# Kernel optimization log

Measured on AMD Instinct MI355X. Metric: run time of the kernel, lower is better.

The kernel has to match this reference:

```python
import jax, jax.numpy as jnp
import numpy as np

NEG_SLOPE = 0.2  # PyG GATConv default LeakyReLU slope


def gat_layer(x, src, dst, W, a_src, a_dst, bias, heads, out_dim, concat, n_nodes):
    # x: [N, F_in]; W: [F_in, heads*out_dim]
    h = (x @ W).reshape(n_nodes, heads, out_dim)          # [N, H, C]
    alpha_src = jnp.sum(h * a_src, axis=-1)               # [N, H]
    alpha_dst = jnp.sum(h * a_dst, axis=-1)               # [N, H]
    e = jax.nn.leaky_relu(alpha_src[src] + alpha_dst[dst], NEG_SLOPE)  # [E, H]
    # softmax over edges grouped by destination node (self-loops guarantee nonempty segments)
    m = jax.ops.segment_max(e, dst, num_segments=n_nodes)  # [N, H]
    w = jnp.exp(e - m[dst])
    s = jax.ops.segment_sum(w, dst, num_segments=n_nodes)  # [N, H]
    alpha = w / s[dst]                                     # [E, H]
    msg = h[src] * alpha[:, :, None]                       # [E, H, C]
    out = jax.ops.segment_sum(msg, dst, num_segments=n_nodes)  # [N, H, C]
    if concat:
        out = out.reshape(n_nodes, heads * out_dim)
    else:
        out = out.mean(axis=1)
    return out + bias


def setup_inputs() -> dict:
    key = jax.random.key(0)
    ks = jax.random.split(key, 12)
    N, E = 50000, 600000
    F_IN, OUT = 256, 64
    H1, C1 = 2, 2 * OUT          # conv1: heads=2, per-head dim 128
    F2 = H1 * C1                 # 256
    x = jax.random.normal(ks[0], (N, F_IN), dtype=jnp.float32)
    edge_index = jax.random.randint(ks[1], (2, E), 0, N, dtype=jnp.int64)
    g1 = 1.0 / np.sqrt(F_IN)
    g2 = 1.0 / np.sqrt(F2)
    return {
        "x": x,
        "edge_index": edge_index,
        "W1": jax.random.normal(ks[2], (F_IN, H1 * C1), dtype=jnp.float32) * g1,
        "a1_src": jax.random.normal(ks[3], (H1, C1), dtype=jnp.float32) * g2,
        "a1_dst": jax.random.normal(ks[4], (H1, C1), dtype=jnp.float32) * g2,
        "b1": jnp.zeros((H1 * C1,), dtype=jnp.float32),
        "W2": jax.random.normal(ks[5], (F2, OUT), dtype=jnp.float32) * g2,
        "a2_src": jax.random.normal(ks[6], (1, OUT), dtype=jnp.float32) * 0.1,
        "a2_dst": jax.random.normal(ks[7], (1, OUT), dtype=jnp.float32) * 0.1,
        "b2": jnp.zeros((OUT,), dtype=jnp.float32),
    }


def reference(x, edge_index, W1, a1_src, a1_dst, b1, W2, a2_src, a2_dst, b2):
    N = x.shape[0]
    # add self-loops (PyG GATConv default)
    loops = jnp.arange(N, dtype=edge_index.dtype)
    src = jnp.concatenate([edge_index[0], loops])
    dst = jnp.concatenate([edge_index[1], loops])
    OUT = W2.shape[1]
    h = gat_layer(x, src, dst, W1, a1_src, a1_dst, b1,
                  heads=2, out_dim=2 * OUT, concat=True, n_nodes=N)
    h = jax.nn.elu(h)
    out = gat_layer(h, src, dst, W2, a2_src, a2_dst, b2,
                    heads=1, out_dim=OUT, concat=False, n_nodes=N)
    return out
```

## Files before the change

kernel.cpp:

```cpp
#include <hip/hip_runtime.h>
#include <hip/hip_bf16.h>
#include <math.h>


#define NSLOPE 0.2f

using bf16x8 = __attribute__((ext_vector_type(8))) short;
using f32x4  = __attribute__((ext_vector_type(4))) float;
using u16x8  = __attribute__((ext_vector_type(8))) unsigned short;
using u16x4  = __attribute__((ext_vector_type(4))) unsigned short;

__device__ __forceinline__ unsigned short bf16_rne(float f) {
    unsigned u = __float_as_uint(f);
    return (unsigned short)((u + 0x7FFFu + ((u >> 16) & 1u)) >> 16);
}
__device__ __forceinline__ float bf16_to_f(unsigned short h) {
    return __uint_as_float(((unsigned)h) << 16);
}

__global__ __launch_bounds__(256) void k_prep_all(const float* __restrict__ x,
                                                  const float* __restrict__ W1,
                                                  const float* __restrict__ W2,
                                                  const int* __restrict__ edst,
                                                  unsigned short* __restrict__ Xhi,
                                                  unsigned short* __restrict__ W1hi,
                                                  unsigned short* __restrict__ W2hi,
                                                  int* __restrict__ deg,
                                                  int BX, int total4, int E) {
    int b = blockIdx.x, t = threadIdx.x;
    if (b < BX) {
        int id = b * 256 + t;
        if (id >= total4) return;
        float4 v = *(const float4*)&x[(size_t)id * 4];
        unsigned short hi[4];
        hi[0] = bf16_rne(v.x); hi[1] = bf16_rne(v.y);
        hi[2] = bf16_rne(v.z); hi[3] = bf16_rne(v.w);
        *(u16x4*)&Xhi[(size_t)id * 4] = *(u16x4*)hi;
    } else if (b < BX + 64) {
        int id = (b - BX) * 256 + t;
        int n = id >> 6, kg = id & 63;
        unsigned short hi[4];
#pragma unroll
        for (int c = 0; c < 4; ++c) {
            float w = W1[(kg * 4 + c) * 256 + n];
            hi[c] = bf16_rne(w);
        }
        *(u16x4*)&W1hi[n * 256 + kg * 4] = *(u16x4*)hi;
    } else if (b < BX + 128) {
        int id = (b - BX - 64) * 256 + t;
        int n = id >> 8, k = id & 255;
        W2hi[n * 256 + k] = bf16_rne(W2[k * 64 + n]);
    } else {
        int i = (b - BX - 128) * 256 + t;
        if (i < E) atomicAdd(&deg[edst[i]], 1);
    }
}

__global__ __launch_bounds__(256) void k_scan_ab(const int* __restrict__ deg,
                                                 int* __restrict__ part,
                                                 int* __restrict__ ticket,
                                                 int* __restrict__ off_n,
                                                 int n, int CH) {
    __shared__ int sd[256];
    __shared__ int lastflag;
    int b = blockIdx.x, t = threadIdx.x;
    int s = b * CH, e = min(n, s + CH);
    int loc = 0;
    for (int i = s + t; i < e; i += 256) loc += deg[i] + 1;
    sd[t] = loc;
    __syncthreads();
    for (int o = 128; o > 0; o >>= 1) {
        if (t < o) sd[t] += sd[t + o];
        __syncthreads();
    }
    if (t == 0) {
        part[b] = sd[0];
        __threadfence();
        int old = atomicAdd(ticket, 1);
        lastflag = (old == (int)gridDim.x - 1);
    }
    __syncthreads();
    if (lastflag) {
        __threadfence();
        int v = ((volatile int*)part)[t];
        sd[t] = v;
        __syncthreads();
        for (int o = 1; o < 256; o <<= 1) {
            int u = (t >= o) ? sd[t - o] : 0;
            __syncthreads();
            sd[t] += u;
            __syncthreads();
        }
        part[t] = sd[t] - v;
        if (t == 255) *off_n = sd[255];
    }
}

__global__ __launch_bounds__(256) void k_scan_c(const int* __restrict__ deg,
                                                const int* __restrict__ part,
                                                int* __restrict__ off,
                                                int* __restrict__ cur,
                                                int* __restrict__ srcl, int n, int CH) {
    __shared__ int sd[256];
    int b = blockIdx.x, t = threadIdx.x;
    int s = b * CH, e = min(n, s + CH);
    int base = part[b];
    for (int c = s; c < e; c += 256) {
        int i = c + t;
        int v = (i < e) ? (deg[i] + 1) : 0;
        sd[t] = v;
        __syncthreads();
        for (int o = 1; o < 256; o <<= 1) {
            int u = (t >= o) ? sd[t - o] : 0;
            __syncthreads();
            sd[t] += u;
            __syncthreads();
        }
        if (i < e) {
            int ex = base + sd[t] - v;
            off[i] = ex;
            cur[i] = ex + 1;
            srcl[ex] = i;
        }
        base += sd[255];
        __syncthreads();
    }
}

__global__ void k_fill(const int* __restrict__ src, const int* __restrict__ dst,
                       int* cur, int* __restrict__ srcl, int E) {
    int i = blockIdx.x * blockDim.x + threadIdx.x;
    if (i >= E) return;
    int s = src[i], d = dst[i];
    int p = atomicAdd(&cur[d], 1);
    srcl[p] = s;
}

#define G1S 40
__global__ __launch_bounds__(256) void k_gemm1(const unsigned short* __restrict__ Xhi,
                                               const unsigned short* __restrict__ Whi,
                                               const float* __restrict__ a1s,
                                               const float* __restrict__ a1d,
                                               unsigned short* __restrict__ h1b,
                                               float* __restrict__ as_,
                                               float* __restrict__ ad_, int M) {
    __shared__ unsigned short sAh[128 * G1S];
    __shared__ unsigned short sBh[128 * G1S];
    __shared__ float salS[128][2], salD[128][2];
    int t = threadIdx.x;
    int lane = t & 63, wave = t >> 6;
    int q = lane >> 4, m = lane & 15;
    int row0 = blockIdx.x * 128;
    int head = blockIdx.y;
    int col0 = head * 128;
    int rbase = (wave & 1) * 64, cbase = (wave >> 1) * 64;
    f32x4 acc[4][4];
#pragma unroll
    for (int i = 0; i < 4; ++i)
#pragma unroll
        for (int j = 0; j < 4; ++j) acc[i][j] = (f32x4){0.f, 0.f, 0.f, 0.f};

    for (int kc = 0; kc < 256; kc += 32) {
#pragma unroll
        for (int i2 = 0; i2 < 2; ++i2) {
            int slot = t + i2 * 256;
            int r = slot >> 2, kg = slot & 3;
            int row = row0 + r;
            u16x8 vh = {0, 0, 0, 0, 0, 0, 0, 0};
            if (row < M) vh = *(const u16x8*)&Xhi[(size_t)row * 256 + kc + kg * 8];
            *(u16x8*)&sAh[r * G1S + kg * 8] = vh;
        }
#pragma unroll
        for (int i2 = 0; i2 < 2; ++i2) {
            int slot = t + i2 * 256;
            int n = slot >> 2, kg = slot & 3;
            *(u16x8*)&sBh[n * G1S + kg * 8] =
                *(const u16x8*)&Whi[(size_t)(col0 + n) * 256 + kc + kg * 8];
        }
        __syncthreads();
        bf16x8 ah[4], bh[4];
#pragma unroll
        for (int i = 0; i < 4; ++i)
            ah[i] = *(bf16x8*)&sAh[(rbase + i * 16 + m) * G1S + q * 8];
#pragma unroll
        for (int j = 0; j < 4; ++j)
            bh[j] = *(bf16x8*)&sBh[(cbase + j * 16 + m) * G1S + q * 8];
#pragma unroll
        for (int i = 0; i < 4; ++i)
#pragma unroll
            for (int j = 0; j < 4; ++j)
                acc[i][j] = __builtin_amdgcn_mfma_f32_16x16x32_bf16(ah[i], bh[j], acc[i][j], 0, 0, 0);
        __syncthreads();
    }
    float sv[4], dv[4];
#pragma unroll
    for (int j = 0; j < 4; ++j) {
        sv[j] = a1s[head * 128 + cbase + j * 16 + m];
        dv[j] = a1d[head * 128 + cbase + j * 16 + m];
    }
#pragma unroll
    for (int i = 0; i < 4; ++i) {
#pragma unroll
        for (int r = 0; r < 4; ++r) {
            int rl = rbase + i * 16 + q * 4 + r;
            int row = row0 + rl;
            float ps = acc[i][0][r] * sv[0] + acc[i][1][r] * sv[1]
                     + acc[i][2][r] * sv[2] + acc[i][3][r] * sv[3];
            float pd = acc[i][0][r] * dv[0] + acc[i][1][r] * dv[1]
                     + acc[i][2][r] * dv[2] + acc[i][3][r] * dv[3];
#pragma unroll
            for (int mask = 1; mask < 16; mask <<= 1) {
                ps += __shfl_xor(ps, mask, 64);
                pd += __shfl_xor(pd, mask, 64);
            }
            if (m == 0) {
                salS[rl][cbase >> 6] = ps;
                salD[rl][cbase >> 6] = pd;
            }
            if (row < M) {
#pragma unroll
                for (int j = 0; j < 4; ++j)
                    h1b[(size_t)row * 256 + col0 + cbase + j * 16 + m] = bf16_rne(acc[i][j][r]);
            }
        }
    }
    __syncthreads();
    if (t < 128) {
        int row = row0 + t;
        if (row < M) {
            as_[row * 2 + head] = salS[t][0] + salS[t][1];
            ad_[row * 2 + head] = salD[t][0] + salD[t][1];
        }
    }
}

__global__ __launch_bounds__(256) void k_agg1(const unsigned short* __restrict__ h1b,
                                              const float* __restrict__ as,
                                              const float* __restrict__ ad,
                                              const int* __restrict__ off,
                                              const int* __restrict__ srcl,
                                              const float* __restrict__ b1,
                                              unsigned short* __restrict__ helu_b, int N) {
    int wid = (blockIdx.x * blockDim.x + threadIdx.x) >> 6;
    int lane = threadIdx.x & 63;
    if (wid >= N) return;
    int p0 = off[wid], p1 = off[wid + 1];
    float ad0 = ad[wid * 2], ad1 = ad[wid * 2 + 1];
    int half = lane >> 5, hl = lane & 31;
    int headL = hl >> 4;
    float acc[8];
#pragma unroll
    for (int c = 0; c < 8; ++c) acc[c] = 0.f;
    float sumw = 0.f;
    for (int base = p0; base < p1; base += 64) {
        int p = base + lane;
        int cnt = min(64, p1 - base);
        int s = 0; float w0 = 0.f, w1 = 0.f;
        if (p < p1) {
            s = srcl[p];
            float2 av = *(const float2*)&as[s * 2];
            float l0 = av.x + ad0; l0 = l0 >= 0.f ? l0 : NSLOPE * l0;
            float l1 = av.y + ad1; l1 = l1 >= 0.f ? l1 : NSLOPE * l1;
            w0 = __expf(l0); w1 = __expf(l1);
        }
        int pairs = (cnt + 1) >> 1;
        int jj = 0;
        for (; jj + 2 <= pairs; jj += 2) {
            int e0 = 2 * jj + half, e1 = e0 + 2;
            int sa = __shfl(s, e0, 64), sb = __shfl(s, e1, 64);
            float wa0 = __shfl(w0, e0, 64), wa1 = __shfl(w1, e0, 64);
            float wb0 = __shfl(w0, e1, 64), wb1 = __shfl(w1, e1, 64);
            u16x8 hva = *(const u16x8*)&h1b[(size_t)sa * 256 + hl * 8];
            u16x8 hvb = *(const u16x8*)&h1b[(size_t)sb * 256 + hl * 8];
            float wa = headL ? wa1 : wa0;
            float wb = headL ? wb1 : wb0;
            sumw += wa + wb;
#pragma unroll
            for (int c = 0; c < 8; ++c)
                acc[c] += wa * bf16_to_f(hva[c]) + wb * bf16_to_f(hvb[c]);
        }
        for (; jj < pairs; ++jj) {
            int e0 = 2 * jj + half;
            int sa = __shfl(s, e0, 64);
            float wa0 = __shfl(w0, e0, 64), wa1 = __shfl(w1, e0, 64);
            u16x8 hva = *(const u16x8*)&h1b[(size_t)sa * 256 + hl * 8];
            float wa = headL ? wa1 : wa0;
            sumw += wa;
#pragma unroll
            for (int c = 0; c < 8; ++c) acc[c] += wa * bf16_to_f(hva[c]);
        }
    }
#pragma unroll
    for (int c = 0; c < 8; ++c) acc[c] += __shfl_xor(acc[c], 32, 64);
    sumw += __shfl_xor(sumw, 32, 64);
    float inv = 1.0f / sumw;
    int ch = hl * 8 + half * 4;
    float4 bv = *(const float4*)&b1[ch];
    float bb[4] = {bv.x, bv.y, bv.z, bv.w};
    unsigned short o[4];
#pragma unroll
    for (int c = 0; c < 4; ++c) {
        float v = acc[half * 4 + c] * inv + bb[c];
        v = v > 0.f ? v : expm1f(v);
        o[c] = bf16_rne(v);
    }
    *(u16x4*)&helu_b[(size_t)wid * 256 + ch] = *(u16x4*)o;
}

__global__ __launch_bounds__(256) void k_gemm2(const unsigned short* __restrict__ hb,
                                               const unsigned short* __restrict__ Whi,
                                               const float* __restrict__ a2s,
                                               const float* __restrict__ a2d,
                                               unsigned short* __restrict__ h2b,
                                               float* __restrict__ as_,
                                               float* __restrict__ ad_, int M) {
    __shared__ unsigned short sA[128 * G1S];
    __shared__ unsigned short sBh[64 * G1S];
    int t = threadIdx.x;
    int lane = t & 63, wave = t >> 6;
    int q = lane >> 4, m = lane & 15;
    int row0 = blockIdx.x * 128;
    int rbase = wave * 32;
    f32x4 acc[2][4];
#pragma unroll
    for (int i = 0; i < 2; ++i)
#pragma unroll
        for (int j = 0; j < 4; ++j) acc[i][j] = (f32x4){0.f, 0.f, 0.f, 0.f};

    for (int kc = 0; kc < 256; kc += 32) {
#pragma unroll
        for (int i = 0; i < 2; ++i) {
            int slot = t + i * 256;
            int r = slot >> 2, kg = slot & 3;
            int row = row0 + r;
            u16x8 v = {0, 0, 0, 0, 0, 0, 0, 0};
            if (row < M) v = *(const u16x8*)&hb[(size_t)row * 256 + kc + kg * 8];
            *(u16x8*)&sA[r * G1S + kg * 8] = v;
        }
        {
            int n = t >> 2, kg = t & 3;
            *(u16x8*)&sBh[n * G1S + kg * 8] =
                *(const u16x8*)&Whi[(size_t)n * 256 + kc + kg * 8];
        }
        __syncthreads();
        bf16x8 a[2], bh[4];
#pragma unroll
        for (int i = 0; i < 2; ++i)
            a[i] = *(bf16x8*)&sA[(rbase + i * 16 + m) * G1S + q * 8];
#pragma unroll
        for (int j = 0; j < 4; ++j)
            bh[j] = *(bf16x8*)&sBh[(j * 16 + m) * G1S + q * 8];
#pragma unroll
        for (int i = 0; i < 2; ++i)
#pragma unroll
            for (int j = 0; j < 4; ++j)
                acc[i][j] = __builtin_amdgcn_mfma_f32_16x16x32_bf16(a[i], bh[j], acc[i][j], 0, 0, 0);
        __syncthreads();
    }
    float sv[4], dv[4];
#pragma unroll
    for (int j = 0; j < 4; ++j) {
        sv[j] = a2s[j * 16 + m];
        dv[j] = a2d[j * 16 + m];
    }
#pragma unroll
    for (int i = 0; i < 2; ++i) {
#pragma unroll
        for (int r = 0; r < 4; ++r) {
            int row = row0 + rbase + i * 16 + q * 4 + r;
            float ps = acc[i][0][r] * sv[0] + acc[i][1][r] * sv[1]
                     + acc[i][2][r] * sv[2] + acc[i][3][r] * sv[3];
            float pd = acc[i][0][r] * dv[0] + acc[i][1][r] * dv[1]
                     + acc[i][2][r] * dv[2] + acc[i][3][r] * dv[3];
#pragma unroll
            for (int mask = 1; mask < 16; mask <<= 1) {
                ps += __shfl_xor(ps, mask, 64);
                pd += __shfl_xor(pd, mask, 64);
            }
            if (row < M) {
#pragma unroll
                for (int j = 0; j < 4; ++j)
                    h2b[(size_t)row * 64 + j * 16 + m] = bf16_rne(acc[i][j][r]);
                if (m == 0) { as_[row] = ps; ad_[row] = pd; }
            }
        }
    }
}

__global__ __launch_bounds__(256) void k_agg2(const unsigned short* __restrict__ h2b,
                                              const float* __restrict__ as,
                                              const float* __restrict__ ad,
                                              const int* __restrict__ off,
                                              const int* __restrict__ srcl,
                                              const float* __restrict__ b2,
                                              float* __restrict__ out, int N) {
    int wid = (blockIdx.x * blockDim.x + threadIdx.x) >> 6;
    int lane = threadIdx.x & 63;
    if (wid >= N) return;
    int p0 = off[wid], p1 = off[wid + 1];
    float adw = ad[wid];
    int g = lane >> 4, gl = lane & 15;
    float acc[4];
#pragma unroll
    for (int c = 0; c < 4; ++c) acc[c] = 0.f;
    float sumw = 0.f;
    for (int base = p0; base < p1; base += 64) {
        int p = base + lane;
        int cnt = min(64, p1 - base);
        int s = 0; float w = 0.f;
        if (p < p1) {
            s = srcl[p];
            float l = as[s] + adw;
            l = l >= 0.f ? l : NSLOPE * l;
            w = __expf(l);
        }
        int quads = (cnt + 3) >> 2;
        int jj = 0;
        for (; jj + 2 <= quads; jj += 2) {
            int e0 = 4 * jj + g, e1 = e0 + 4;
            int sa = __shfl(s, e0, 64), sb = __shfl(s, e1, 64);
            float wa = __shfl(w, e0, 64), wb = __shfl(w, e1, 64);
            u16x4 hva = *(const u16x4*)&h2b[(size_t)sa * 64 + gl * 4];
            u16x4 hvb = *(const u16x4*)&h2b[(size_t)sb * 64 + gl * 4];
            sumw += wa + wb;
            acc[0] += wa * bf16_to_f(hva.x) + wb * bf16_to_f(hvb.x);
            acc[1] += wa * bf16_to_f(hva.y) + wb * bf16_to_f(hvb.y);
            acc[2] += wa * bf16_to_f(hva.z) + wb * bf16_to_f(hvb.z);
            acc[3] += wa * bf16_to_f(hva.w) + wb * bf16_to_f(hvb.w);
        }
        for (; jj < quads; ++jj) {
            int e0 = 4 * jj + g;
            int sa = __shfl(s, e0, 64);
            float wa = __shfl(w, e0, 64);
            u16x4 hva = *(const u16x4*)&h2b[(size_t)sa * 64 + gl * 4];
            sumw += wa;
            acc[0] += wa * bf16_to_f(hva.x);
            acc[1] += wa * bf16_to_f(hva.y);
            acc[2] += wa * bf16_to_f(hva.z);
            acc[3] += wa * bf16_to_f(hva.w);
        }
    }
#pragma unroll
    for (int c = 0; c < 4; ++c) {
        acc[c] += __shfl_xor(acc[c], 16, 64);
        acc[c] += __shfl_xor(acc[c], 32, 64);
    }
    sumw += __shfl_xor(sumw, 16, 64);
    sumw += __shfl_xor(sumw, 32, 64);
    if (g == 0) {
        float inv = 1.0f / sumw;
        float4 bv = *(const float4*)&b2[gl * 4];
        float4 o;
        o.x = acc[0] * inv + bv.x;
        o.y = acc[1] * inv + bv.y;
        o.z = acc[2] * inv + bv.z;
        o.w = acc[3] * inv + bv.w;
        *(float4*)&out[(size_t)wid * 64 + gl * 4] = o;
    }
}

extern "C" void kernel_launch(void* const* d_in, const int* in_sizes, int n_in,
                              void* d_out, int out_size, void* d_ws, size_t ws_size,
                              hipStream_t stream) {
    if (n_in < 10) return;
    const float* x   = (const float*)d_in[0];
    const int*   ei  = (const int*)d_in[1];
    const float* W1  = (const float*)d_in[2];
    const float* a1s = (const float*)d_in[3];
    const float* a1d = (const float*)d_in[4];
    const float* b1  = (const float*)d_in[5];
    const float* W2  = (const float*)d_in[6];
    const float* a2s = (const float*)d_in[7];
    const float* a2d = (const float*)d_in[8];
    const float* b2  = (const float*)d_in[9];
    float* out = (float*)d_out;

    const int N = in_sizes[0] / 256;
    const int E = in_sizes[1] / 2;
    const int T = E + N;
    const int* esrc = ei;
    const int* edst = ei + E;

    char* ws = (char*)d_ws;
    size_t o = 0;
    auto alloc = [&](size_t bytes) -> void* {
        void* p = ws + o;
        o = (o + bytes + 255) & ~(size_t)255;
        return p;
    };
    size_t szX = (size_t)N * 256 * 2;
    char* regionA = (char*)alloc(szX);
    unsigned short* Xhi    = (unsigned short*)regionA;
    unsigned short* helu_b = (unsigned short*)regionA;

    unsigned short* h1b  = (unsigned short*)alloc((size_t)N * 256 * 2);
    unsigned short* W1hi = (unsigned short*)alloc(256 * 256 * 2);
    unsigned short* W2hi = (unsigned short*)alloc(64 * 256 * 2);
    unsigned short* h2b  = (unsigned short*)alloc((size_t)N * 64 * 2);
    float* al1s = (float*)alloc((size_t)N * 2 * 4);
    float* al1d = (float*)alloc((size_t)N * 2 * 4);
    float* al2s = (float*)alloc((size_t)N * 4);
    float* al2d = (float*)alloc((size_t)N * 4);
    int* deg  = (int*)alloc((size_t)(N + 64) * 4);
    int* ticket = deg + N;
    int* off  = (int*)alloc((size_t)(N + 1) * 4);
    int* cur  = (int*)alloc((size_t)N * 4);
    int* part = (int*)alloc(256 * 4);
    int* srcl = (int*)alloc((size_t)T * 4);
    if (o > ws_size) return;

    const int CH = (N + 255) / 256;
    const int total4 = N * 64;
    const int BX = (total4 + 255) / 256;
    const int BH = (E + 255) / 256;

    hipMemsetAsync(deg, 0, (size_t)(N + 64) * 4, stream);
    k_prep_all<<<BX + 128 + BH, 256, 0, stream>>>(x, W1, W2, edst, Xhi,
                                                  W1hi, W2hi, deg,
                                                  BX, total4, E);
    k_scan_ab<<<256, 256, 0, stream>>>(deg, part, ticket, &off[N], N, CH);
    k_scan_c<<<256, 256, 0, stream>>>(deg, part, off, cur, srcl, N, CH);
    k_fill<<<(E + 255) / 256, 256, 0, stream>>>(esrc, edst, cur, srcl, E);

    dim3 g1((N + 127) / 128, 2);
    k_gemm1<<<g1, 256, 0, stream>>>(Xhi, W1hi, a1s, a1d, h1b, al1s, al1d, N);
    k_agg1<<<(N + 3) / 4, 256, 0, stream>>>(h1b, al1s, al1d, off, srcl, b1, helu_b, N);

    k_gemm2<<<(N + 127) / 128, 256, 0, stream>>>(helu_b, W2hi, a2s, a2d,
                                                 h2b, al2s, al2d, N);
    k_agg2<<<(N + 3) / 4, 256, 0, stream>>>(h2b, al2s, al2d, off, srcl, b2, out, N);
}
```

Baseline: 287.7 us.

## Fuse graph preprocessing stages into one cooperative kernel with grid syncs

Replaces the memset, prep, two-phase scan and fill kernels with a single cooperative kernel of 1024 blocks that uses grid-wide barriers between stages. The goal is to cut launch overhead and inter-kernel gaps in the CSR build. In exchange, each stage runs grid-stride loops on a fixed grid and pays for grid syncs, and the block-level scan phases use only 256 of the 1024 blocks.

```diff
diff --git a/kernel.cpp b/kernel.cpp
--- a/kernel.cpp
+++ b/kernel.cpp
@@ -1,6 +1,9 @@
 #include <hip/hip_runtime.h>
 #include <hip/hip_bf16.h>
+#include <hip/hip_cooperative_groups.h>
 #include <math.h>
+
+namespace cg = cooperative_groups;
 
 
 #define NSLOPE 0.2f
@@ -18,72 +21,67 @@
     return __uint_as_float(((unsigned)h) << 16);
 }
 
-__global__ __launch_bounds__(256) void k_prep_all(const float* __restrict__ x,
-                                                  const float* __restrict__ W1,
-                                                  const float* __restrict__ W2,
-                                                  const int* __restrict__ edst,
-                                                  unsigned short* __restrict__ Xhi,
-                                                  unsigned short* __restrict__ W1hi,
-                                                  unsigned short* __restrict__ W2hi,
-                                                  int* __restrict__ deg,
-                                                  int BX, int total4, int E) {
+__global__ __launch_bounds__(256) void k_graph(const float* __restrict__ x,
+                                               const float* __restrict__ W1,
+                                               const float* __restrict__ W2,
+                                               const int* __restrict__ esrc,
+                                               const int* __restrict__ edst,
+                                               unsigned short* __restrict__ Xhi,
+                                               unsigned short* __restrict__ W1hi,
+                                               unsigned short* __restrict__ W2hi,
+                                               int* __restrict__ deg,
+                                               int* __restrict__ part,
+                                               int* __restrict__ off,
+                                               int* __restrict__ cur,
+                                               int* __restrict__ srcl,
+                                               int N, int E, int total4, int CH) {
+    cg::grid_group gg = cg::this_grid();
+    __shared__ int sd[256];
     int b = blockIdx.x, t = threadIdx.x;
-    if (b < BX) {
-        int id = b * 256 + t;
-        if (id >= total4) return;
+    int tid = b * 256 + t;
+    int nthr = gridDim.x * 256;
+
+    for (int i = tid; i < N; i += nthr) deg[i] = 0;
+    for (int id = tid; id < total4; id += nthr) {
         float4 v = *(const float4*)&x[(size_t)id * 4];
         unsigned short hi[4];
         hi[0] = bf16_rne(v.x); hi[1] = bf16_rne(v.y);
         hi[2] = bf16_rne(v.z); hi[3] = bf16_rne(v.w);
         *(u16x4*)&Xhi[(size_t)id * 4] = *(u16x4*)hi;
-    } else if (b < BX + 64) {
-        int id = (b - BX) * 256 + t;
+    }
+    for (int id = tid; id < 16384; id += nthr) {
         int n = id >> 6, kg = id & 63;
         unsigned short hi[4];
 #pragma unroll
-        for (int c = 0; c < 4; ++c) {
-            float w = W1[(kg * 4 + c) * 256 + n];
-            hi[c] = bf16_rne(w);
-        }
+        for (int c = 0; c < 4; ++c) hi[c] = bf16_rne(W1[(kg * 4 + c) * 256 + n]);
         *(u16x4*)&W1hi[n * 256 + kg * 4] = *(u16x4*)hi;
-    } else if (b < BX + 128) {
-        int id = (b - BX - 64) * 256 + t;
+    }
+    for (int id = tid; id < 16384; id += nthr) {
         int n = id >> 8, k = id & 255;
         W2hi[n * 256 + k] = bf16_rne(W2[k * 64 + n]);
-    } else {
-        int i = (b - BX - 128) * 256 + t;
-        if (i < E) atomicAdd(&deg[edst[i]], 1);
-    }
-}
-
-__global__ __launch_bounds__(256) void k_scan_ab(const int* __restrict__ deg,
-                                                 int* __restrict__ part,
-                                                 int* __restrict__ ticket,
-                                                 int* __restrict__ off_n,
-                                                 int n, int CH) {
-    __shared__ int sd[256];
-    __shared__ int lastflag;
-    int b = blockIdx.x, t = threadIdx.x;
-    int s = b * CH, e = min(n, s + CH);
-    int loc = 0;
-    for (int i = s + t; i < e; i += 256) loc += deg[i] + 1;
-    sd[t] = loc;
-    __syncthreads();
-    for (int o = 128; o > 0; o >>= 1) {
-        if (t < o) sd[t] += sd[t + o];
-        __syncthreads();
-    }
-    if (t == 0) {
-        part[b] = sd[0];
-        __threadfence();
-        int old = atomicAdd(ticket, 1);
-        lastflag = (old == (int)gridDim.x - 1);
-    }
-    __syncthreads();
-    if (lastflag) {
-        __threadfence();
-        int v = ((volatile int*)part)[t];
-        sd[t] = v;
+    }
+    gg.sync();
+
+    for (int i = tid; i < E; i += nthr) atomicAdd(&deg[edst[i]], 1);
+    gg.sync();
+
+    if (b < 256) {
+        int s = b * CH, e = min(N, s + CH);
+        int loc = 0;
+        for (int i = s + t; i < e; i += 256) loc += deg[i] + 1;
+        sd[t] = loc;
+        __syncthreads();
+        for (int o = 128; o > 0; o >>= 1) {
+            if (t < o) sd[t] += sd[t + o];
+            __syncthreads();
+        }
+        if (t == 0) part[b] = sd[0];
+    }
+    gg.sync();
+
+    if (b < 256) {
+        int pb = part[b];
+        sd[t] = part[t];
         __syncthreads();
         for (int o = 1; o < 256; o <<= 1) {
             int u = (t >= o) ? sd[t - o] : 0;
@@ -91,49 +89,38 @@
             sd[t] += u;
             __syncthreads();
         }
-        part[t] = sd[t] - v;
-        if (t == 255) *off_n = sd[255];
-    }
-}
-
-__global__ __launch_bounds__(256) void k_scan_c(const int* __restrict__ deg,
-                                                const int* __restrict__ part,
-                                                int* __restrict__ off,
-                                                int* __restrict__ cur,
-                                                int* __restrict__ srcl, int n, int CH) {
-    __shared__ int sd[256];
-    int b = blockIdx.x, t = threadIdx.x;
-    int s = b * CH, e = min(n, s + CH);
-    int base = part[b];
-    for (int c = s; c < e; c += 256) {
-        int i = c + t;
-        int v = (i < e) ? (deg[i] + 1) : 0;
-        sd[t] = v;
-        __syncthreads();
-        for (int o = 1; o < 256; o <<= 1) {
-            int u = (t >= o) ? sd[t - o] : 0;
+        int base = sd[b] - pb;
+        if (b == 0 && t == 0) off[N] = sd[255];
+        __syncthreads();
+        int s = b * CH, e = min(N, s + CH);
+        for (int c = s; c < e; c += 256) {
+            int i = c + t;
+            int vv = (i < e) ? (deg[i] + 1) : 0;
+            sd[t] = vv;
             __syncthreads();
-            sd[t] += u;
+            for (int o = 1; o < 256; o <<= 1) {
+                int u = (t >= o) ? sd[t - o] : 0;
+                __syncthreads();
+                sd[t] += u;
+                __syncthreads();
+            }
+            if (i < e) {
+                int ex = base + sd[t] - vv;
+                off[i] = ex;
+                cur[i] = ex + 1;
+                srcl[ex] = i;
+            }
+            base += sd[255];
             __syncthreads();
         }
-        if (i < e) {
-            int ex = base + sd[t] - v;
-            off[i] = ex;
-            cur[i] = ex + 1;
-            srcl[ex] = i;
-        }
-        base += sd[255];
-        __syncthreads();
-    }
-}
-
-__global__ void k_fill(const int* __restrict__ src, const int* __restrict__ dst,
-                       int* cur, int* __restrict__ srcl, int E) {
-    int i = blockIdx.x * blockDim.x + threadIdx.x;
-    if (i >= E) return;
-    int s = src[i], d = dst[i];
-    int p = atomicAdd(&cur[d], 1);
-    srcl[p] = s;
+    }
+    gg.sync();
+
+    for (int i = tid; i < E; i += nthr) {
+        int s = esrc[i], d = edst[i];
+        int p = atomicAdd(&cur[d], 1);
+        srcl[p] = s;
+    }
 }
 
 #define G1S 40
@@ -502,7 +489,6 @@
     float* al2s = (float*)alloc((size_t)N * 4);
     float* al2d = (float*)alloc((size_t)N * 4);
     int* deg  = (int*)alloc((size_t)(N + 64) * 4);
-    int* ticket = deg + N;
     int* off  = (int*)alloc((size_t)(N + 1) * 4);
     int* cur  = (int*)alloc((size_t)N * 4);
     int* part = (int*)alloc(256 * 4);
@@ -511,16 +497,16 @@
 
     const int CH = (N + 255) / 256;
     const int total4 = N * 64;
-    const int BX = (total4 + 255) / 256;
-    const int BH = (E + 255) / 256;
-
-    hipMemsetAsync(deg, 0, (size_t)(N + 64) * 4, stream);
-    k_prep_all<<<BX + 128 + BH, 256, 0, stream>>>(x, W1, W2, edst, Xhi,
-                                                  W1hi, W2hi, deg,
-                                                  BX, total4, E);
-    k_scan_ab<<<256, 256, 0, stream>>>(deg, part, ticket, &off[N], N, CH);
-    k_scan_c<<<256, 256, 0, stream>>>(deg, part, off, cur, srcl, N, CH);
-    k_fill<<<(E + 255) / 256, 256, 0, stream>>>(esrc, edst, cur, srcl, E);
+
+    {
+        int N_ = N, E_ = E, total4_ = total4, CH_ = CH;
+        void* args[] = {(void*)&x, (void*)&W1, (void*)&W2, (void*)&esrc, (void*)&edst,
+                        (void*)&Xhi, (void*)&W1hi, (void*)&W2hi,
+                        (void*)&deg, (void*)&part, (void*)&off, (void*)&cur, (void*)&srcl,
+                        (void*)&N_, (void*)&E_, (void*)&total4_, (void*)&CH_};
+        hipLaunchCooperativeKernel((const void*)k_graph, dim3(1024), dim3(256),
+                                   args, 0, stream);
+    }
 
     dim3 g1((N + 127) / 128, 2);
     k_gemm1<<<g1, 256, 0, stream>>>(Xhi, W1hi, a1s, a1d, h1b, al1s, al1d, N);
```

After: 717.2 us. 149% more time.

## Fuse CSR scan and edge fill into one kernel with grid barriers

Applied to the files above, without the earlier changes.

Merges the three CSR-building kernels (block partial sums, offset scan, edge fill) into a single persistent 256-block kernel that uses a software grid barrier built on an atomic counter between phases. Each block redoes the small 256-entry prefix scan itself instead of relying on a last-block ticket. The goal is to cut two kernel launches and their inter-kernel gaps. In exchange, correctness depends on all 256 blocks being co-resident, and the fill phase now runs a grid-stride loop over edges with only 65536 threads.

```diff
diff --git a/kernel.cpp b/kernel.cpp
--- a/kernel.cpp
+++ b/kernel.cpp
@@ -56,15 +56,31 @@
     }
 }
 
-__global__ __launch_bounds__(256) void k_scan_ab(const int* __restrict__ deg,
-                                                 int* __restrict__ part,
-                                                 int* __restrict__ ticket,
-                                                 int* __restrict__ off_n,
-                                                 int n, int CH) {
+__device__ __forceinline__ void gbar256(int* bar, int phase) {
+    __syncthreads();
+    if (threadIdx.x == 0) {
+        __hip_atomic_fetch_add(bar, 1, __ATOMIC_ACQ_REL, __HIP_MEMORY_SCOPE_AGENT);
+        while (__hip_atomic_load(bar, __ATOMIC_ACQUIRE, __HIP_MEMORY_SCOPE_AGENT)
+               < 256 * phase) {
+            __builtin_amdgcn_s_sleep(8);
+        }
+    }
+    __syncthreads();
+}
+
+__global__ __launch_bounds__(256) void k_scanfill(const int* __restrict__ deg,
+                                                  const int* __restrict__ esrc,
+                                                  const int* __restrict__ edst,
+                                                  int* __restrict__ part,
+                                                  int* __restrict__ bar,
+                                                  int* __restrict__ off,
+                                                  int* __restrict__ cur,
+                                                  int* __restrict__ srcl,
+                                                  int N, int E, int CH) {
     __shared__ int sd[256];
-    __shared__ int lastflag;
     int b = blockIdx.x, t = threadIdx.x;
-    int s = b * CH, e = min(n, s + CH);
+    int s = b * CH, e = min(N, s + CH);
+
     int loc = 0;
     for (int i = s + t; i < e; i += 256) loc += deg[i] + 1;
     sd[t] = loc;
@@ -73,17 +89,35 @@
         if (t < o) sd[t] += sd[t + o];
         __syncthreads();
     }
-    if (t == 0) {
-        part[b] = sd[0];
-        __threadfence();
-        int old = atomicAdd(ticket, 1);
-        lastflag = (old == (int)gridDim.x - 1);
-    }
-    __syncthreads();
-    if (lastflag) {
-        __threadfence();
-        int v = ((volatile int*)part)[t];
-        sd[t] = v;
+    if (t == 0)
+        __hip_atomic_store(&part[b], sd[0], __ATOMIC_RELEASE, __HIP_MEMORY_SCOPE_AGENT);
+    gbar256(bar, 1);
+
+    int pb = __hip_atomic_load(&part[t], __ATOMIC_ACQUIRE, __HIP_MEMORY_SCOPE_AGENT);
+    sd[t] = pb;
+    __syncthreads();
+    for (int o = 1; o < 256; o <<= 1) {
+        int u = (t >= o) ? sd[t - o] : 0;
+        __syncthreads();
+        sd[t] += u;
+        __syncthreads();
+    }
+    int base = sd[b];
+    int total = sd[255];
+    __syncthreads();
+    if (t == 0) sd[0] = base;
+    __syncthreads();
+    int own;
+    {
+        own = __hip_atomic_load(&part[b], __ATOMIC_ACQUIRE, __HIP_MEMORY_SCOPE_AGENT);
+    }
+    base = sd[0] - own;
+    if (b == 0 && t == 0) off[N] = total;
+    __syncthreads();
+    for (int c = s; c < e; c += 256) {
+        int i = c + t;
+        int vv = (i < e) ? (deg[i] + 1) : 0;
+        sd[t] = vv;
         __syncthreads();
         for (int o = 1; o < 256; o <<= 1) {
             int u = (t >= o) ? sd[t - o] : 0;
@@ -91,33 +125,8 @@
             sd[t] += u;
             __syncthreads();
         }
-        part[t] = sd[t] - v;
-        if (t == 255) *off_n = sd[255];
-    }
-}
-
-__global__ __launch_bounds__(256) void k_scan_c(const int* __restrict__ deg,
-                                                const int* __restrict__ part,
-                                                int* __restrict__ off,
-                                                int* __restrict__ cur,
-                                                int* __restrict__ srcl, int n, int CH) {
-    __shared__ int sd[256];
-    int b = blockIdx.x, t = threadIdx.x;
-    int s = b * CH, e = min(n, s + CH);
-    int base = part[b];
-    for (int c = s; c < e; c += 256) {
-        int i = c + t;
-        int v = (i < e) ? (deg[i] + 1) : 0;
-        sd[t] = v;
-        __syncthreads();
-        for (int o = 1; o < 256; o <<= 1) {
-            int u = (t >= o) ? sd[t - o] : 0;
-            __syncthreads();
-            sd[t] += u;
-            __syncthreads();
-        }
         if (i < e) {
-            int ex = base + sd[t] - v;
+            int ex = base + sd[t] - vv;
             off[i] = ex;
             cur[i] = ex + 1;
             srcl[ex] = i;
@@ -125,15 +134,14 @@
         base += sd[255];
         __syncthreads();
     }
-}
-
-__global__ void k_fill(const int* __restrict__ src, const int* __restrict__ dst,
-                       int* cur, int* __restrict__ srcl, int E) {
-    int i = blockIdx.x * blockDim.x + threadIdx.x;
-    if (i >= E) return;
-    int s = src[i], d = dst[i];
-    int p = atomicAdd(&cur[d], 1);
-    srcl[p] = s;
+    gbar256(bar, 2);
+
+    int tid = b * 256 + t, nthr = 256 * 256;
+    for (int i = tid; i < E; i += nthr) {
+        int ss = esrc[i], d = edst[i];
+        int p = atomicAdd(&cur[d], 1);
+        srcl[p] = ss;
+    }
 }
 
 #define G1S 40
@@ -502,7 +510,7 @@
     float* al2s = (float*)alloc((size_t)N * 4);
     float* al2d = (float*)alloc((size_t)N * 4);
     int* deg  = (int*)alloc((size_t)(N + 64) * 4);
-    int* ticket = deg + N;
+    int* bar  = deg + N;
     int* off  = (int*)alloc((size_t)(N + 1) * 4);
     int* cur  = (int*)alloc((size_t)N * 4);
     int* part = (int*)alloc(256 * 4);
@@ -518,9 +526,8 @@
     k_prep_all<<<BX + 128 + BH, 256, 0, stream>>>(x, W1, W2, edst, Xhi,
                                                   W1hi, W2hi, deg,
                                                   BX, total4, E);
-    k_scan_ab<<<256, 256, 0, stream>>>(deg, part, ticket, &off[N], N, CH);
-    k_scan_c<<<256, 256, 0, stream>>>(deg, part, off, cur, srcl, N, CH);
-    k_fill<<<(E + 255) / 256, 256, 0, stream>>>(esrc, edst, cur, srcl, E);
+    k_scanfill<<<256, 256, 0, stream>>>(deg, esrc, edst, part, bar,
+                                        off, cur, srcl, N, E, CH);
 
     dim3 g1((N + 127) / 128, 2);
     k_gemm1<<<g1, 256, 0, stream>>>(Xhi, W1hi, a1s, a1d, h1b, al1s, al1d, N);
```

Result: slower. 328.5 us (+14.2%).

## Compute both heads per GEMM1 block and unroll aggregation loops by four

Applied to the files above, without the earlier changes.

GEMM1 now computes all 256 output columns (both heads) in one block, with each wave covering 64 rows by 128 columns of one head. This halves the grid, avoids reading the X tile twice, and drops the cross-wave sum of attention logits. The cost is a doubled accumulator array (128 floats per lane) and larger B staging in LDS, which raises register pressure and may lower occupancy. Both aggregation kernels also gain a 4-edge unrolled gather loop so more independent row loads are in flight.

```diff
diff --git a/kernel.cpp b/kernel.cpp
--- a/kernel.cpp
+++ b/kernel.cpp
@@ -145,20 +145,20 @@
                                                float* __restrict__ as_,
                                                float* __restrict__ ad_, int M) {
     __shared__ unsigned short sAh[128 * G1S];
-    __shared__ unsigned short sBh[128 * G1S];
+    __shared__ unsigned short sBh[256 * G1S];
     __shared__ float salS[128][2], salD[128][2];
     int t = threadIdx.x;
     int lane = t & 63, wave = t >> 6;
     int q = lane >> 4, m = lane & 15;
     int row0 = blockIdx.x * 128;
-    int head = blockIdx.y;
-    int col0 = head * 128;
-    int rbase = (wave & 1) * 64, cbase = (wave >> 1) * 64;
-    f32x4 acc[4][4];
+    int rbase = (wave & 1) * 64;
+    int head = wave >> 1;
+    int cbase = head * 128;
+    f32x4 acc[4][8];
 #pragma unroll
     for (int i = 0; i < 4; ++i)
 #pragma unroll
-        for (int j = 0; j < 4; ++j) acc[i][j] = (f32x4){0.f, 0.f, 0.f, 0.f};
+        for (int j = 0; j < 8; ++j) acc[i][j] = (f32x4){0.f, 0.f, 0.f, 0.f};
 
     for (int kc = 0; kc < 256; kc += 32) {
 #pragma unroll
@@ -171,32 +171,32 @@
             *(u16x8*)&sAh[r * G1S + kg * 8] = vh;
         }
 #pragma unroll
-        for (int i2 = 0; i2 < 2; ++i2) {
+        for (int i2 = 0; i2 < 4; ++i2) {
             int slot = t + i2 * 256;
             int n = slot >> 2, kg = slot & 3;
             *(u16x8*)&sBh[n * G1S + kg * 8] =
-                *(const u16x8*)&Whi[(size_t)(col0 + n) * 256 + kc + kg * 8];
-        }
-        __syncthreads();
-        bf16x8 ah[4], bh[4];
+                *(const u16x8*)&Whi[(size_t)n * 256 + kc + kg * 8];
+        }
+        __syncthreads();
+        bf16x8 ah[4], bh[8];
 #pragma unroll
         for (int i = 0; i < 4; ++i)
             ah[i] = *(bf16x8*)&sAh[(rbase + i * 16 + m) * G1S + q * 8];
 #pragma unroll
-        for (int j = 0; j < 4; ++j)
+        for (int j = 0; j < 8; ++j)
             bh[j] = *(bf16x8*)&sBh[(cbase + j * 16 + m) * G1S + q * 8];
 #pragma unroll
         for (int i = 0; i < 4; ++i)
 #pragma unroll
-            for (int j = 0; j < 4; ++j)
+            for (int j = 0; j < 8; ++j)
                 acc[i][j] = __builtin_amdgcn_mfma_f32_16x16x32_bf16(ah[i], bh[j], acc[i][j], 0, 0, 0);
         __syncthreads();
     }
-    float sv[4], dv[4];
-#pragma unroll
-    for (int j = 0; j < 4; ++j) {
-        sv[j] = a1s[head * 128 + cbase + j * 16 + m];
-        dv[j] = a1d[head * 128 + cbase + j * 16 + m];
+    float sv[8], dv[8];
+#pragma unroll
+    for (int j = 0; j < 8; ++j) {
+        sv[j] = a1s[cbase + j * 16 + m];
+        dv[j] = a1d[cbase + j * 16 + m];
     }
 #pragma unroll
     for (int i = 0; i < 4; ++i) {
@@ -204,23 +204,25 @@
         for (int r = 0; r < 4; ++r) {
             int rl = rbase + i * 16 + q * 4 + r;
             int row = row0 + rl;
-            float ps = acc[i][0][r] * sv[0] + acc[i][1][r] * sv[1]
-                     + acc[i][2][r] * sv[2] + acc[i][3][r] * sv[3];
-            float pd = acc[i][0][r] * dv[0] + acc[i][1][r] * dv[1]
-                     + acc[i][2][r] * dv[2] + acc[i][3][r] * dv[3];
+            float ps = 0.f, pd = 0.f;
+#pragma unroll
+            for (int j = 0; j < 8; ++j) {
+                ps += acc[i][j][r] * sv[j];
+                pd += acc[i][j][r] * dv[j];
+            }
 #pragma unroll
             for (int mask = 1; mask < 16; mask <<= 1) {
                 ps += __shfl_xor(ps, mask, 64);
                 pd += __shfl_xor(pd, mask, 64);
             }
             if (m == 0) {
-                salS[rl][cbase >> 6] = ps;
-                salD[rl][cbase >> 6] = pd;
+                salS[rl][head] = ps;
+                salD[rl][head] = pd;
             }
             if (row < M) {
 #pragma unroll
-                for (int j = 0; j < 4; ++j)
-                    h1b[(size_t)row * 256 + col0 + cbase + j * 16 + m] = bf16_rne(acc[i][j][r]);
+                for (int j = 0; j < 8; ++j)
+                    h1b[(size_t)row * 256 + cbase + j * 16 + m] = bf16_rne(acc[i][j][r]);
             }
         }
     }
@@ -228,8 +230,10 @@
     if (t < 128) {
         int row = row0 + t;
         if (row < M) {
-            as_[row * 2 + head] = salS[t][0] + salS[t][1];
-            ad_[row * 2 + head] = salD[t][0] + salD[t][1];
+            as_[row * 2 + 0] = salS[t][0];
+            as_[row * 2 + 1] = salS[t][1];
+            ad_[row * 2 + 0] = salD[t][0];
+            ad_[row * 2 + 1] = salD[t][1];
         }
     }
 }
@@ -265,6 +269,28 @@
         }
         int pairs = (cnt + 1) >> 1;
         int jj = 0;
+        for (; jj + 4 <= pairs; jj += 4) {
+            int e0 = 2 * jj + half, e1 = e0 + 2, e2 = e0 + 4, e3 = e0 + 6;
+            int sa = __shfl(s, e0, 64), sb = __shfl(s, e1, 64);
+            int sc = __shfl(s, e2, 64), se = __shfl(s, e3, 64);
+            float wa0 = __shfl(w0, e0, 64), wa1 = __shfl(w1, e0, 64);
+            float wb0 = __shfl(w0, e1, 64), wb1 = __shfl(w1, e1, 64);
+            float wc0 = __shfl(w0, e2, 64), wc1 = __shfl(w1, e2, 64);
+            float wd0 = __shfl(w0, e3, 64), wd1 = __shfl(w1, e3, 64);
+            u16x8 hva = *(const u16x8*)&h1b[(size_t)sa * 256 + hl * 8];
+            u16x8 hvb = *(const u16x8*)&h1b[(size_t)sb * 256 + hl * 8];
+            u16x8 hvc = *(const u16x8*)&h1b[(size_t)sc * 256 + hl * 8];
+            u16x8 hvd = *(const u16x8*)&h1b[(size_t)se * 256 + hl * 8];
+            float wa = headL ? wa1 : wa0;
+            float wb = headL ? wb1 : wb0;
+            float wc = headL ? wc1 : wc0;
+            float wd = headL ? wd1 : wd0;
+            sumw += (wa + wb) + (wc + wd);
+#pragma unroll
+            for (int c = 0; c < 8; ++c)
+                acc[c] += (wa * bf16_to_f(hva[c]) + wb * bf16_to_f(hvb[c]))
+                        + (wc * bf16_to_f(hvc[c]) + wd * bf16_to_f(hvd[c]));
+        }
         for (; jj + 2 <= pairs; jj += 2) {
             int e0 = 2 * jj + half, e1 = e0 + 2;
             int sa = __shfl(s, e0, 64), sb = __shfl(s, e1, 64);
@@ -416,6 +442,26 @@
         }
         int quads = (cnt + 3) >> 2;
         int jj = 0;
+        for (; jj + 4 <= quads; jj += 4) {
+            int e0 = 4 * jj + g, e1 = e0 + 4, e2 = e0 + 8, e3 = e0 + 12;
+            int sa = __shfl(s, e0, 64), sb = __shfl(s, e1, 64);
+            int sc = __shfl(s, e2, 64), se = __shfl(s, e3, 64);
+            float wa = __shfl(w, e0, 64), wb = __shfl(w, e1, 64);
+            float wc = __shfl(w, e2, 64), wd = __shfl(w, e3, 64);
+            u16x4 hva = *(const u16x4*)&h2b[(size_t)sa * 64 + gl * 4];
+            u16x4 hvb = *(const u16x4*)&h2b[(size_t)sb * 64 + gl * 4];
+            u16x4 hvc = *(const u16x4*)&h2b[(size_t)sc * 64 + gl * 4];
+            u16x4 hvd = *(const u16x4*)&h2b[(size_t)se * 64 + gl * 4];
+            sumw += (wa + wb) + (wc + wd);
+            acc[0] += (wa * bf16_to_f(hva.x) + wb * bf16_to_f(hvb.x))
+                    + (wc * bf16_to_f(hvc.x) + wd * bf16_to_f(hvd.x));
+            acc[1] += (wa * bf16_to_f(hva.y) + wb * bf16_to_f(hvb.y))
+                    + (wc * bf16_to_f(hvc.y) + wd * bf16_to_f(hvd.y));
+            acc[2] += (wa * bf16_to_f(hva.z) + wb * bf16_to_f(hvb.z))
+                    + (wc * bf16_to_f(hvc.z) + wd * bf16_to_f(hvd.z));
+            acc[3] += (wa * bf16_to_f(hva.w) + wb * bf16_to_f(hvb.w))
+                    + (wc * bf16_to_f(hvc.w) + wd * bf16_to_f(hvd.w));
+        }
         for (; jj + 2 <= quads; jj += 2) {
             int e0 = 4 * jj + g, e1 = e0 + 4;
             int sa = __shfl(s, e0, 64), sb = __shfl(s, e1, 64);
@@ -522,8 +568,7 @@
     k_scan_c<<<256, 256, 0, stream>>>(deg, part, off, cur, srcl, N, CH);
     k_fill<<<(E + 255) / 256, 256, 0, stream>>>(esrc, edst, cur, srcl, E);
 
-    dim3 g1((N + 127) / 128, 2);
-    k_gemm1<<<g1, 256, 0, stream>>>(Xhi, W1hi, a1s, a1d, h1b, al1s, al1d, N);
+    k_gemm1<<<(N + 127) / 128, 256, 0, stream>>>(Xhi, W1hi, a1s, a1d, h1b, al1s, al1d, N);
     k_agg1<<<(N + 3) / 4, 256, 0, stream>>>(h1b, al1s, al1d, off, srcl, b1, helu_b, N);
 
     k_gemm2<<<(N + 127) / 128, 256, 0, stream>>>(helu_b, W2hi, a2s, a2d,
```

Result: no change. 288.3 us (+0.2%).
